# Optimization experiments

Hardware: AMD Instinct MI355X
Metric: run time of the kernel (lower is better)

Reference implementation:

```python
import jax, jax.numpy as jnp
import numpy as np

PAD_IDX = 0
EPS = 1e-5


def make_pos(L):
    # phrase[i, j] = j - i, i.e. row i is range(-i, L-i)
    phrase = (np.arange(L)[None, :] - np.arange(L)[:, None]).astype(np.float32)
    half = int(np.ceil(L / 2))
    freq = np.linspace(0.0, L, L, dtype=np.float32)[1:half]          # [F]
    pos = freq[:, None, None] * phrase[None] / L * 2.0 * np.pi       # [F, L, L]
    pos = np.concatenate([np.cos(pos), np.sin(pos)], axis=0)        # [2F, L, L]
    return jnp.asarray(np.transpose(pos, (1, 0, 2)))                # [L, P=2F, L]


def setup_inputs() -> dict:
    key = jax.random.key(0)
    ks = jax.random.split(key, 8)
    B, L, V, D, H = 2048, 64, 4096, 64, 8
    P = 2 * (int(np.ceil(L / 2)) - 1)  # 62
    inputs = jax.random.randint(ks[0], (B, L), 0, V)
    W_emb = jax.random.normal(ks[1], (V, D), jnp.float32) * 0.02
    W_emb = W_emb.at[PAD_IDX].set(0.0)  # padding_idx row is zero
    W_qkv = jax.random.normal(ks[2], (3 * H * D, D), jnp.float32) * 0.02
    W_pos = jax.random.normal(ks[3], (P, L), jnp.float32) * 0.02
    ln_g = jnp.ones((D,), jnp.float32)
    ln_b = jnp.zeros((D,), jnp.float32)
    W1 = jax.random.normal(ks[4], (64, H), jnp.float32) * 0.1
    b1 = jnp.zeros((64,), jnp.float32)
    W2 = jax.random.normal(ks[5], (32, 64), jnp.float32) * 0.1
    b2 = jnp.zeros((32,), jnp.float32)
    return dict(inputs=inputs, W_emb=W_emb, W_qkv=W_qkv, W_pos=W_pos,
                ln_g=ln_g, ln_b=ln_b, W1=W1, b1=b1, W2=W2, b2=b2,
                n_words=4, n_names=16)


def reference(inputs, W_emb, W_qkv, W_pos, ln_g, ln_b, W1, b1, W2, b2, n_words, n_names):
    B, L = inputs.shape
    V, D = W_emb.shape
    H = W_qkv.shape[0] // (3 * D)
    pos = make_pos(L)  # [L, P, L]
    P = pos.shape[1]

    # compute_qkv: per-char q/k/v tables, then gather per token.
    qkv = (W_emb @ W_qkv.T).reshape(V, 3 * H, D)
    q, k, v = qkv[:, :H], qkv[:, H:2 * H], qkv[:, 2 * H:]
    q_t = jnp.take(q, inputs, axis=0)  # [B, L, H, D]
    k_t = jnp.take(k, inputs, axis=0)
    v_t = jnp.take(v, inputs, axis=0)

    # Equivalent to gathering char_sim[h, ids, ids]: qkv is a per-token linear,
    # so q[ids] @ k[ids]^T == char_sim.index_select(1, ids).index_select(-1, ids).
    sim = jnp.einsum('blhd,bmhd->bhlm', q_t, k_t) / jnp.sqrt(jnp.float32(D))
    key_pad = (inputs == PAD_IDX)[:, None, None, :]
    sim = jnp.where(key_pad, jnp.float32(-1e9), sim)  # char_sim[:, :, pad_idx] = -1e9

    # positional bias: Linear(L->P) on clipped scores, contracted with pos basis.
    sim_clip = jnp.where(sim > -1e8, sim, jnp.float32(0.0))
    pos_w = jnp.einsum('bhlm,pm->bhlp', sim_clip, W_pos)        # [B, H, L, P]
    pos_bias = jnp.einsum('bhlp,lpm->bhlm', pos_w, pos) / P     # mean over P

    attn = jax.nn.softmax(sim + pos_bias, axis=-1)              # dropout p=0 -> id
    out = jnp.einsum('bhlm,bmhd->blhd', attn, v_t)              # [B, L, H, D]

    # sdpa LayerNorm over word_vec_d
    mu = out.mean(-1, keepdims=True)
    var = out.var(-1, keepdims=True)
    out = (out - mu) * jax.lax.rsqrt(var + EPS) * ln_g + ln_b

    # MLP over the head dimension: [B, L, D, H] -> [B, L, D, 32]
    ft = jnp.swapaxes(out, 2, 3)
    h1 = jax.nn.relu(jnp.einsum('bldh,oh->bldo', ft, W1) + b1)
    h2 = jnp.einsum('bldo,po->bldp', h1, W2) + b2
    char_ft = h2.reshape(B, L, -1)                              # [B, L, D*32]

    # masked mean pooling over chars -> word feature
    maskf = (inputs != PAD_IDX).astype(char_ft.dtype)
    word_ft = jnp.einsum('bl,blf->bf', maskf, char_ft) / maskf.sum(-1, keepdims=True)

    # equal-size splits: words -> names (mean) -> groups of names
    Fdim = word_ft.shape[-1]
    name_ft = word_ft.reshape(B // n_words, n_words, Fdim).mean(1)
    return name_ft.reshape(-1, n_names, Fdim)
```

## Files before the change

kernel.cpp:

```cpp
#include <hip/hip_runtime.h>
#include <hip/hip_bf16.h>


typedef __attribute__((ext_vector_type(8))) short short8;
typedef __attribute__((ext_vector_type(4))) float f32x4;

union FragU { uint4 u; short8 v; };

__device__ __forceinline__ unsigned short f2bf(float f) {
    union { float f; unsigned int i; } c; c.f = f;
    unsigned int i = c.i;
    unsigned int r = (i + 0x7fffu + ((i >> 16) & 1u)) >> 16;
    return (unsigned short)r;
}
__device__ __forceinline__ float asf(unsigned int u) {
    union { unsigned int i; float f; } c; c.i = u; return c.f;
}
__device__ __forceinline__ float bfsel(uint2 g, int i) {
    unsigned u = (i < 2) ? g.x : g.y;
    return asf((i & 1) ? (u & 0xffff0000u) : (u << 16));
}
__device__ __forceinline__ unsigned cvtpk(float lo, float hi) {
    unsigned r;
    asm("v_cvt_pk_bf16_f32 %0, %1, %2" : "=v"(r) : "v"(lo), "v"(hi));
    return r;
}

__device__ __forceinline__ void packstore4(unsigned* rowptr, int c,
                                           float v0, float v1, float v2, float v3) {
    float p0 = __shfl_xor(v0, 1), p1 = __shfl_xor(v1, 1);
    float p2 = __shfl_xor(v2, 1), p3 = __shfl_xor(v3, 1);
    int odd = c & 1;
    float lo0 = odd ? p2 : v0, hi0 = odd ? v2 : p0;
    float lo1 = odd ? p3 : v1, hi1 = odd ? v3 : p1;
    unsigned a0 = cvtpk(lo0, hi0);
    unsigned a1 = cvtpk(lo1, hi1);
    int ba = (c >> 1) + (odd ? 16 : 0);
    rowptr[ba] = a0; rowptr[ba + 8] = a1;
}

__device__ __forceinline__ void packline(unsigned* rowbase, int c,
                                         float v0, float v1, float v2, float v3) {
    float p0 = __shfl_xor(v0, 1), p1 = __shfl_xor(v1, 1);
    float p2 = __shfl_xor(v2, 1), p3 = __shfl_xor(v3, 1);
    int odd = c & 1;
    float lo0 = odd ? p2 : v0, hi0 = odd ? v2 : p0;
    float lo1 = odd ? p3 : v1, hi1 = odd ? v3 : p1;
    unsigned a0 = cvtpk(lo0, hi0);
    unsigned a1 = cvtpk(lo1, hi1);
    int s = (c >> 1) + (odd ? 8 : 0);
    rowbase[s] = a0; rowbase[s + 16] = a1;
}

__global__ __launch_bounds__(256) void k_qkv(const float* __restrict__ W_emb,
                                             const float* __restrict__ W_qkv,
                                             unsigned short* __restrict__ qkvb) {
    __shared__ float At[4096];
    __shared__ float Bt[4096];
    int t = threadIdx.x;
    int bt = blockIdx.x / 24, rt = blockIdx.x - bt * 24;
    int r = t >> 2, part = t & 3;
    const float4* esrc = (const float4*)(W_emb + (size_t)((bt << 6) + r) * 64 + part * 16);
    const float4* wsrc = (const float4*)(W_qkv + (size_t)((rt << 6) + r) * 64 + part * 16);
#pragma unroll
    for (int j = 0; j < 4; ++j) {
        float4 e4 = esrc[j], w4 = wsrc[j];
        int c0 = part * 16 + j * 4;
        At[(c0 + 0) * 64 + r] = e4.x; At[(c0 + 1) * 64 + r] = e4.y;
        At[(c0 + 2) * 64 + r] = e4.z; At[(c0 + 3) * 64 + r] = e4.w;
        Bt[(c0 + 0) * 64 + r] = w4.x; Bt[(c0 + 1) * 64 + r] = w4.y;
        Bt[(c0 + 2) * 64 + r] = w4.z; Bt[(c0 + 3) * 64 + r] = w4.w;
    }
    __syncthreads();
    int l0 = (t >> 4) << 2, m0 = (t & 15) << 2;
    float acc[4][4] = {};
#pragma unroll 4
    for (int k = 0; k < 64; ++k) {
        float4 a  = *(const float4*)(At + k * 64 + l0);
        float4 bb = *(const float4*)(Bt + k * 64 + m0);
        float aa[4] = {a.x, a.y, a.z, a.w};
        float bv[4] = {bb.x, bb.y, bb.z, bb.w};
#pragma unroll
        for (int i = 0; i < 4; ++i)
#pragma unroll
            for (int j = 0; j < 4; ++j)
                acc[i][j] = fmaf(aa[i], bv[j], acc[i][j]);
    }
    float qs = (rt < 8) ? 0.18033688f : 1.0f;
#pragma unroll
    for (int i = 0; i < 4; ++i) {
        unsigned w0 = (unsigned)f2bf(acc[i][0] * qs) | ((unsigned)f2bf(acc[i][1] * qs) << 16);
        unsigned w1 = (unsigned)f2bf(acc[i][2] * qs) | ((unsigned)f2bf(acc[i][3] * qs) << 16);
        unsigned* dst = (unsigned*)(qkvb + (size_t)((bt << 6) + l0 + i) * 1536 + (rt << 6) + m0);
        dst[0] = w0; dst[1] = w1;
    }
}

__global__ void k_tab(const float* __restrict__ W_pos,
                      unsigned short* __restrict__ cst,
                      unsigned short* __restrict__ csl,
                      unsigned short* __restrict__ wpos) {
    int t = threadIdx.x;
    const float w = 6.283185307179586f / 63.0f;
    for (int e = t; e < 4096; e += 256) {
        int row = e >> 6, col = e & 63;
        {
            int j = col, x = row;
            float val = 0.0f;
            if (j < 31)       val = cosf(w * (float)(((j + 1) * x) % 63));
            else if (j >= 32 && j < 63) val = sinf(w * (float)(((j - 31) * x) % 63));
            cst[e] = f2bf(val);
        }
        {
            int j = row, x = col;
            float val = 0.0f;
            if (j < 31)       val = cosf(w * (float)(((j + 1) * x) % 63));
            else if (j >= 32 && j < 63) val = sinf(w * (float)(((j - 31) * x) % 63));
            csl[e] = f2bf(val);
        }
        {
            int j = row;
            float val = 0.0f;
            if (j < 31) val = W_pos[j * 64 + col];
            else if (j >= 32 && j < 63) val = W_pos[(j - 1) * 64 + col];
            wpos[e] = f2bf(val);
        }
    }
}

__global__ __launch_bounds__(128, 4) void k_attn(
    const int* __restrict__ inputs,
    const unsigned short* __restrict__ qkvb,
    const unsigned short* __restrict__ cstg,
    const unsigned short* __restrict__ cslg,
    const unsigned short* __restrict__ wposg,
    const float* __restrict__ ln_g,
    const float* __restrict__ ln_b,
    unsigned short* __restrict__ out_n)
{
    __shared__ __align__(16) unsigned int smem[4608];
    unsigned int* S0d = smem;
    unsigned int* S1d = smem + 2304;
    int t = threadIdx.x, w2 = t >> 6, lane = t & 63;
    int b = blockIdx.x >> 3, h = blockIdx.x & 7;
    const int* toks = inputs + b * 64;
    int r = lane & 15, q = lane >> 4, c = r;
    int tk = toks[lane];
    int mt0 = 2 * w2;
    const float INV62 = 1.0f / 62.0f;

    int mk[4]; float gvv[4], bvv[4];
#pragma unroll
    for (int nt = 0; nt < 4; ++nt) {
        mk[nt] = (toks[16 * nt + c] == 0);
        gvv[nt] = ln_g[16 * nt + c];
        bvv[nt] = ln_b[16 * nt + c];
    }

    {
        const uint4* src = (const uint4*)(qkvb + (size_t)tk * 1536 + (w2 ? 512 : 0) + h * 64);
        uint4* dst = (uint4*)((w2 ? S1d : S0d) + lane * 36);
#pragma unroll
        for (int j = 0; j < 8; ++j) dst[j] = src[j];
    }
    __syncthreads();

    f32x4 sc[2][4], acc[2][4];
    const f32x4 zf = {0.f, 0.f, 0.f, 0.f};

#pragma unroll
    for (int u = 0; u < 2; ++u)
#pragma unroll
        for (int nt = 0; nt < 4; ++nt) sc[u][nt] = zf;
#pragma unroll
    for (int ks = 0; ks < 2; ++ks) {
        FragU Af[2], Bf[4];
#pragma unroll
        for (int u = 0; u < 2; ++u)
            Af[u].u = *(const uint4*)(S0d + (16 * (mt0 + u) + r) * 36 + 16 * ks + 4 * q);
#pragma unroll
        for (int nt = 0; nt < 4; ++nt)
            Bf[nt].u = *(const uint4*)(S1d + (16 * nt + r) * 36 + 16 * ks + 4 * q);
#pragma unroll
        for (int u = 0; u < 2; ++u)
#pragma unroll
            for (int nt = 0; nt < 4; ++nt)
                sc[u][nt] = __builtin_amdgcn_mfma_f32_16x16x32_bf16(Af[u].v, Bf[nt].v, sc[u][nt], 0, 0, 0);
    }
#pragma unroll
    for (int u = 0; u < 2; ++u)
#pragma unroll
        for (int i = 0; i < 4; ++i) {
            int l = 16 * (mt0 + u) + 4 * q + i;
            packstore4(S0d + l * 36, c, sc[u][0][i], sc[u][1][i], sc[u][2][i], sc[u][3][i]);
        }
    __syncthreads();

#pragma unroll
    for (int u = 0; u < 2; ++u)
#pragma unroll
        for (int nt = 0; nt < 4; ++nt) acc[u][nt] = zf;
#pragma unroll
    for (int ks = 0; ks < 2; ++ks) {
        FragU Af[2], Bf[4];
#pragma unroll
        for (int u = 0; u < 2; ++u)
            Af[u].u = *(const uint4*)(S0d + (16 * (mt0 + u) + r) * 36 + 16 * ks + 4 * q);
#pragma unroll
        for (int nt = 0; nt < 4; ++nt)
            Bf[nt].u = *(const uint4*)(wposg + (16 * nt + r) * 64 + 32 * ks + 8 * q);
#pragma unroll
        for (int u = 0; u < 2; ++u)
#pragma unroll
            for (int nt = 0; nt < 4; ++nt)
                acc[u][nt] = __builtin_amdgcn_mfma_f32_16x16x32_bf16(Af[u].v, Bf[nt].v, acc[u][nt], 0, 0, 0);
    }
#pragma unroll
    for (int u = 0; u < 2; ++u) {
        int mt = mt0 + u;
        uint2 t00 = *(const uint2*)(cslg + (c) * 64 + 16 * mt + 4 * q);
        uint2 t01 = *(const uint2*)(cslg + (32 + c) * 64 + 16 * mt + 4 * q);
        uint2 t10 = *(const uint2*)(cslg + (16 + c) * 64 + 16 * mt + 4 * q);
        uint2 t11 = *(const uint2*)(cslg + (48 + c) * 64 + 16 * mt + 4 * q);
#pragma unroll
        for (int i = 0; i < 4; ++i) {
            int l = 16 * mt + 4 * q + i;
            float cv0 = bfsel(t00, i), sv0 = bfsel(t01, i);
            float cv1 = bfsel(t10, i), sv1 = bfsel(t11, i);
            float pc0 = acc[u][0][i], ps0 = acc[u][2][i];
            float pc1 = acc[u][1][i], ps1 = acc[u][3][i];
            float u0 = pc0 * cv0 - ps0 * sv0;
            float u1 = pc1 * cv1 - ps1 * sv1;
            float u2 = pc0 * sv0 + ps0 * cv0;
            float u3 = pc1 * sv1 + ps1 * cv1;
            packstore4(S1d + l * 36, c, u0, u1, u2, u3);
        }
    }

#pragma unroll
    for (int u = 0; u < 2; ++u)
#pragma unroll
        for (int nt = 0; nt < 4; ++nt) acc[u][nt] = zf;
#pragma unroll
    for (int ks = 0; ks < 2; ++ks) {
        FragU Af[2], Bf[4];
#pragma unroll
        for (int u = 0; u < 2; ++u)
            Af[u].u = *(const uint4*)(S1d + (16 * (mt0 + u) + r) * 36 + 16 * ks + 4 * q);
#pragma unroll
        for (int nt = 0; nt < 4; ++nt)
            Bf[nt].u = *(const uint4*)(cstg + (16 * nt + r) * 64 + 32 * ks + 8 * q);
#pragma unroll
        for (int u = 0; u < 2; ++u)
#pragma unroll
            for (int nt = 0; nt < 4; ++nt)
                acc[u][nt] = __builtin_amdgcn_mfma_f32_16x16x32_bf16(Af[u].v, Bf[nt].v, acc[u][nt], 0, 0, 0);
    }

    uint4 V4[4];
    {
        const uint4* vsrc = (const uint4*)(qkvb + (size_t)tk * 1536 + 1024 + h * 64 + 32 * w2);
#pragma unroll
        for (int j = 0; j < 4; ++j) V4[j] = vsrc[j];
    }

#pragma unroll
    for (int u = 0; u < 2; ++u)
#pragma unroll
        for (int i = 0; i < 4; ++i) {
            int l = 16 * (mt0 + u) + 4 * q + i;
            float e0 = mk[0] ? 0.f : __builtin_amdgcn_exp2f(fmaf(acc[u][0][i], INV62, sc[u][0][i]));
            float e1 = mk[1] ? 0.f : __builtin_amdgcn_exp2f(fmaf(acc[u][1][i], INV62, sc[u][1][i]));
            float e2 = mk[2] ? 0.f : __builtin_amdgcn_exp2f(fmaf(acc[u][2][i], INV62, sc[u][2][i]));
            float e3 = mk[3] ? 0.f : __builtin_amdgcn_exp2f(fmaf(acc[u][3][i], INV62, sc[u][3][i]));
            float s = e0 + e1 + e2 + e3;
            s += __shfl_xor(s, 1);
            s += __shfl_xor(s, 2);
            s += __shfl_xor(s, 4);
            s += __shfl_xor(s, 8);
            float inv = __builtin_amdgcn_rcpf(s);
            packstore4(S0d + l * 36, c, e0 * inv, e1 * inv, e2 * inv, e3 * inv);
        }

    {
        int odd = lane & 1;
        const unsigned* Vd = (const unsigned*)V4;
#pragma unroll
        for (int jj = 0; jj < 16; ++jj) {
            unsigned my = Vd[jj];
            unsigned pr = __shfl_xor(my, 1);
            unsigned val = odd ? ((pr >> 16) | (my & 0xffff0000u))
                               : ((my & 0xffffu) | (pr << 16));
            S1d[(32 * w2 + 2 * jj + odd) * 36 + (lane >> 1)] = val;
        }
    }
    __syncthreads();

#pragma unroll
    for (int u = 0; u < 2; ++u)
#pragma unroll
        for (int nt = 0; nt < 4; ++nt) acc[u][nt] = zf;
#pragma unroll
    for (int ks = 0; ks < 2; ++ks) {
        FragU Af[2], Bf[4];
#pragma unroll
        for (int u = 0; u < 2; ++u)
            Af[u].u = *(const uint4*)(S0d + (16 * (mt0 + u) + r) * 36 + 16 * ks + 4 * q);
#pragma unroll
        for (int nt = 0; nt < 4; ++nt)
            Bf[nt].u = *(const uint4*)(S1d + (16 * nt + r) * 36 + 16 * ks + 4 * q);
#pragma unroll
        for (int u = 0; u < 2; ++u)
#pragma unroll
            for (int nt = 0; nt < 4; ++nt)
                acc[u][nt] = __builtin_amdgcn_mfma_f32_16x16x32_bf16(Af[u].v, Bf[nt].v, acc[u][nt], 0, 0, 0);
    }
    {
        unsigned* outw = (unsigned*)out_n;
        size_t hb = ((size_t)b * 8 + h) * 64;
#pragma unroll
        for (int u = 0; u < 2; ++u)
#pragma unroll
            for (int i = 0; i < 4; ++i) {
                int l = 16 * (mt0 + u) + 4 * q + i;
                float v0 = acc[u][0][i], v1 = acc[u][1][i], v2 = acc[u][2][i], v3 = acc[u][3][i];
                float s1 = v0 + v1 + v2 + v3;
                float s2 = v0 * v0 + v1 * v1 + v2 * v2 + v3 * v3;
                s1 += __shfl_xor(s1, 1); s2 += __shfl_xor(s2, 1);
                s1 += __shfl_xor(s1, 2); s2 += __shfl_xor(s2, 2);
                s1 += __shfl_xor(s1, 4); s2 += __shfl_xor(s2, 4);
                s1 += __shfl_xor(s1, 8); s2 += __shfl_xor(s2, 8);
                float mu = s1 * (1.0f / 64.0f);
                float var = s2 * (1.0f / 64.0f) - mu * mu;
                float rstd = __builtin_amdgcn_rsqf(var + 1e-5f);
                float cmu = -mu * rstd;
                float y0 = fmaf(fmaf(v0, rstd, cmu), gvv[0], bvv[0]);
                float y1 = fmaf(fmaf(v1, rstd, cmu), gvv[1], bvv[1]);
                float y2 = fmaf(fmaf(v2, rstd, cmu), gvv[2], bvv[2]);
                float y3 = fmaf(fmaf(v3, rstd, cmu), gvv[3], bvv[3]);
                packline(outw + (hb + l) * 32, c, y0, y1, y2, y3);
            }
    }
}

__global__ __launch_bounds__(256) void k_mlp(const int* __restrict__ inputs,
                                             const unsigned short* __restrict__ out_n,
                                             const float* __restrict__ W1,
                                             const float* __restrict__ b1,
                                             float* __restrict__ gws) {
    __shared__ unsigned short XT[8320];
    __shared__ unsigned long long vmask_s;
    __shared__ float invcnt_s;
    int t = threadIdx.x, w = t >> 6, lane = t & 63;
    int b = blockIdx.x;
    int ot = w >> 1, dt = w & 1;
    int kq = lane >> 4, n = lane & 15;

    if (t < 64) {
        int tok = inputs[b * 64 + t];
        unsigned long long bal = __ballot(tok != 0);
        if (t == 0) {
            int cnt = __popcll(bal);
            if (cnt < 1) cnt = 1;
            vmask_s = bal;
            invcnt_s = 1.0f / (float)cnt;
        }
    }

    FragU Wf[2];
#pragma unroll
    for (int om = 0; om < 2; ++om) {
        int o = 32 * ot + 16 * om + n;
        if (kq == 0) {
            const float4* wsrc = (const float4*)(W1 + o * 8);
            float4 wa = wsrc[0], wb = wsrc[1];
            Wf[om].u.x = (unsigned)f2bf(wa.x) | ((unsigned)f2bf(wa.y) << 16);
            Wf[om].u.y = (unsigned)f2bf(wa.z) | ((unsigned)f2bf(wa.w) << 16);
            Wf[om].u.z = (unsigned)f2bf(wb.x) | ((unsigned)f2bf(wb.y) << 16);
            Wf[om].u.w = (unsigned)f2bf(wb.z) | ((unsigned)f2bf(wb.w) << 16);
        } else if (kq == 1) {
            Wf[om].u = make_uint4((unsigned)f2bf(b1[o]), 0, 0, 0);
        } else {
            Wf[om].u = make_uint4(0, 0, 0, 0);
        }
    }

    f32x4 racc[2][2];
    const f32x4 zf = {0.f, 0.f, 0.f, 0.f};
#pragma unroll
    for (int dm = 0; dm < 2; ++dm)
#pragma unroll
        for (int om = 0; om < 2; ++om) racc[dm][om] = zf;

    int lh = t & 7;
    int lr = (t >> 3) & 15;
    int half = t >> 7;

    __syncthreads();
    unsigned long long vmask = vmask_s;
    float invcnt = invcnt_s;

    for (int cc = 0; cc < 4; ++cc) {
        __syncthreads();
        {
            const unsigned short* src = out_n + (size_t)b * 32768 + lh * 4096
                                        + (16 * cc + lr) * 64 + half * 32;
            unsigned short* dst = XT + lr * 520 + lh;
#pragma unroll
            for (int j = 0; j < 4; ++j) {
                uint4 u = ((const uint4*)src)[j];
                int m0 = half * 32 + j * 8;
                int d0 = (m0 >= 16 && m0 < 48) ? (m0 ^ 48) : m0;
                dst[(d0 + 0) * 8] = (unsigned short)(u.x & 0xffffu);
                dst[(d0 + 1) * 8] = (unsigned short)(u.x >> 16);
                dst[(d0 + 2) * 8] = (unsigned short)(u.y & 0xffffu);
                dst[(d0 + 3) * 8] = (unsigned short)(u.y >> 16);
                dst[(d0 + 4) * 8] = (unsigned short)(u.z & 0xffffu);
                dst[(d0 + 5) * 8] = (unsigned short)(u.z >> 16);
                dst[(d0 + 6) * 8] = (unsigned short)(u.w & 0xffffu);
                dst[(d0 + 7) * 8] = (unsigned short)(u.w >> 16);
            }
        }
        __syncthreads();
#pragma unroll 4
        for (int l = 0; l < 16; ++l) {
            if (!((vmask >> (16 * cc + l)) & 1ull)) continue;
            FragU Xf[2];
#pragma unroll
            for (int dm = 0; dm < 2; ++dm) {
                if (kq == 0)
                    Xf[dm].u = *(const uint4*)(XT + l * 520 + (32 * dt + 16 * dm + n) * 8);
                else if (kq == 1)
                    Xf[dm].u = make_uint4(0x3F80u, 0, 0, 0);
                else
                    Xf[dm].u = make_uint4(0, 0, 0, 0);
            }
#pragma unroll
            for (int dm = 0; dm < 2; ++dm)
#pragma unroll
                for (int om = 0; om < 2; ++om) {
                    f32x4 C = __builtin_amdgcn_mfma_f32_16x16x32_bf16(Xf[dm].v, Wf[om].v, zf, 0, 0, 0);
#pragma unroll
                    for (int i = 0; i < 4; ++i)
                        racc[dm][om][i] += fmaxf(C[i], 0.0f);
                }
        }
    }
    float* gb = gws + (size_t)b * 4096;
#pragma unroll
    for (int dm = 0; dm < 2; ++dm)
#pragma unroll
        for (int om = 0; om < 2; ++om) {
            int o = 32 * ot + 16 * om + n;
#pragma unroll
            for (int i = 0; i < 4; ++i) {
                int d = 32 * dt + 16 * dm + 4 * kq + i;
                gb[d * 64 + o] = racc[dm][om][i] * invcnt;
            }
        }
}

__global__ __launch_bounds__(256) void k_final(const float* __restrict__ gws,
                                               const float* __restrict__ W2,
                                               const float* __restrict__ b2,
                                               float* __restrict__ out) {
    __shared__ float gbar[4096];
    __shared__ float w2s[32 * 68];
    __shared__ float b2s[32];
    int t = threadIdx.x;
    int n = blockIdx.x;
    for (int e = t; e < 4096; e += 256) {
        size_t base = (size_t)(4 * n) * 4096 + e;
        gbar[e] = 0.25f * (gws[base] + gws[base + 4096] + gws[base + 8192] + gws[base + 12288]);
    }
    for (int e = t; e < 2048; e += 256) {
        int p = e >> 6, o = e & 63;
        w2s[p * 68 + o] = W2[e];
    }
    if (t < 32) b2s[t] = b2[t];
    __syncthreads();
#pragma unroll
    for (int jj = 0; jj < 8; ++jj) {
        int f = jj * 256 + t;
        int d = f >> 5, p = f & 31;
        float acc = b2s[p];
        for (int o4 = 0; o4 < 16; ++o4) {
            float4 gvv = *(const float4*)(gbar + d * 64 + o4 * 4);
            float4 wv = *(const float4*)(w2s + p * 68 + o4 * 4);
            acc = fmaf(gvv.x, wv.x, acc);
            acc = fmaf(gvv.y, wv.y, acc);
            acc = fmaf(gvv.z, wv.z, acc);
            acc = fmaf(gvv.w, wv.w, acc);
        }
        out[(size_t)n * 2048 + f] = acc;
    }
}

extern "C" void kernel_launch(void* const* d_in, const int* in_sizes, int n_in,
                              void* d_out, int out_size, void* d_ws, size_t ws_size,
                              hipStream_t stream) {
    const int*   inputs = (const int*)d_in[0];
    const float* W_emb  = (const float*)d_in[1];
    const float* W_qkv  = (const float*)d_in[2];
    const float* W_pos  = (const float*)d_in[3];
    const float* ln_g   = (const float*)d_in[4];
    const float* ln_b   = (const float*)d_in[5];
    const float* W1     = (const float*)d_in[6];
    const float* b1     = (const float*)d_in[7];
    const float* W2     = (const float*)d_in[8];
    const float* b2     = (const float*)d_in[9];
    float* out = (float*)d_out;

    unsigned short* qkvb = (unsigned short*)d_ws;
    unsigned short* cst  = qkvb + 6291456;
    unsigned short* csl  = cst + 4096;
    unsigned short* wpos = csl + 4096;
    float* gws = (float*)(wpos + 4096);
    unsigned short* out_n = (unsigned short*)(gws + 8388608);

    hipLaunchKernelGGL(k_qkv,   dim3(64 * 24), dim3(256), 0, stream, W_emb, W_qkv, qkvb);
    hipLaunchKernelGGL(k_tab,   dim3(1),       dim3(256), 0, stream, W_pos, cst, csl, wpos);
    hipLaunchKernelGGL(k_attn,  dim3(16384),   dim3(128), 0, stream,
                       inputs, qkvb, cst, csl, wpos, ln_g, ln_b, out_n);
    hipLaunchKernelGGL(k_mlp,   dim3(2048),    dim3(256), 0, stream, inputs, out_n, W1, b1, gws);
    hipLaunchKernelGGL(k_final, dim3(512),     dim3(256), 0, stream, gws, W2, b2, out);
}
```

Before: 355.8 us.

## Prefetch MLP transpose tiles, pair-pack LDS writes, parallelize table kernel

In the MLP kernel, the next chunk's global loads of normalized attention output are issued into registers before the current chunk's MFMA loop, hiding global latency. The LDS transpose now writes 32-bit words built by exchanging halves with the neighbouring lane via shuffle, instead of eight 16-bit scattered stores. The trig/position table kernel is spread over 16 blocks instead of a single looping block. The prefetch costs extra registers, and the shuffle-based packing depends on the lane-pair mapping being correct.

```diff
diff --git a/kernel.cpp b/kernel.cpp
--- a/kernel.cpp
+++ b/kernel.cpp
@@ -100,31 +100,29 @@
                       unsigned short* __restrict__ cst,
                       unsigned short* __restrict__ csl,
                       unsigned short* __restrict__ wpos) {
-    int t = threadIdx.x;
+    int e = blockIdx.x * 256 + threadIdx.x;
     const float w = 6.283185307179586f / 63.0f;
-    for (int e = t; e < 4096; e += 256) {
-        int row = e >> 6, col = e & 63;
-        {
-            int j = col, x = row;
-            float val = 0.0f;
-            if (j < 31)       val = cosf(w * (float)(((j + 1) * x) % 63));
-            else if (j >= 32 && j < 63) val = sinf(w * (float)(((j - 31) * x) % 63));
-            cst[e] = f2bf(val);
-        }
-        {
-            int j = row, x = col;
-            float val = 0.0f;
-            if (j < 31)       val = cosf(w * (float)(((j + 1) * x) % 63));
-            else if (j >= 32 && j < 63) val = sinf(w * (float)(((j - 31) * x) % 63));
-            csl[e] = f2bf(val);
-        }
-        {
-            int j = row;
-            float val = 0.0f;
-            if (j < 31) val = W_pos[j * 64 + col];
-            else if (j >= 32 && j < 63) val = W_pos[(j - 1) * 64 + col];
-            wpos[e] = f2bf(val);
-        }
+    int row = e >> 6, col = e & 63;
+    {
+        int j = col, x = row;
+        float val = 0.0f;
+        if (j < 31)       val = cosf(w * (float)(((j + 1) * x) % 63));
+        else if (j >= 32 && j < 63) val = sinf(w * (float)(((j - 31) * x) % 63));
+        cst[e] = f2bf(val);
+    }
+    {
+        int j = row, x = col;
+        float val = 0.0f;
+        if (j < 31)       val = cosf(w * (float)(((j + 1) * x) % 63));
+        else if (j >= 32 && j < 63) val = sinf(w * (float)(((j - 31) * x) % 63));
+        csl[e] = f2bf(val);
+    }
+    {
+        int j = row;
+        float val = 0.0f;
+        if (j < 31) val = W_pos[j * 64 + col];
+        else if (j >= 32 && j < 63) val = W_pos[(j - 1) * 64 + col];
+        wpos[e] = f2bf(val);
     }
 }
 
@@ -396,30 +394,39 @@
     int lr = (t >> 3) & 15;
     int half = t >> 7;
 
+    const uint4* src4 = (const uint4*)(out_n + (size_t)b * 32768 + lh * 4096
+                                       + lr * 64 + half * 32);
+    uint4 G[4], Gn[4];
+#pragma unroll
+    for (int j = 0; j < 4; ++j) G[j] = src4[j];
+
+    int c2 = lh >> 1, lodd = lh & 1;
+    unsigned* XTd = (unsigned*)XT;
+    int dbase = lr * 260 + c2;
+
     __syncthreads();
     unsigned long long vmask = vmask_s;
     float invcnt = invcnt_s;
 
     for (int cc = 0; cc < 4; ++cc) {
         __syncthreads();
-        {
-            const unsigned short* src = out_n + (size_t)b * 32768 + lh * 4096
-                                        + (16 * cc + lr) * 64 + half * 32;
-            unsigned short* dst = XT + lr * 520 + lh;
-#pragma unroll
-            for (int j = 0; j < 4; ++j) {
-                uint4 u = ((const uint4*)src)[j];
-                int m0 = half * 32 + j * 8;
-                int d0 = (m0 >= 16 && m0 < 48) ? (m0 ^ 48) : m0;
-                dst[(d0 + 0) * 8] = (unsigned short)(u.x & 0xffffu);
-                dst[(d0 + 1) * 8] = (unsigned short)(u.x >> 16);
-                dst[(d0 + 2) * 8] = (unsigned short)(u.y & 0xffffu);
-                dst[(d0 + 3) * 8] = (unsigned short)(u.y >> 16);
-                dst[(d0 + 4) * 8] = (unsigned short)(u.z & 0xffffu);
-                dst[(d0 + 5) * 8] = (unsigned short)(u.z >> 16);
-                dst[(d0 + 6) * 8] = (unsigned short)(u.w & 0xffffu);
-                dst[(d0 + 7) * 8] = (unsigned short)(u.w >> 16);
+#pragma unroll
+        for (int j = 0; j < 4; ++j) {
+            int m0 = half * 32 + j * 8;
+            int d0 = (m0 >= 16 && m0 < 48) ? (m0 ^ 48) : m0;
+            unsigned wv[4] = {G[j].x, G[j].y, G[j].z, G[j].w};
+#pragma unroll
+            for (int i = 0; i < 4; ++i) {
+                unsigned pw = __shfl_xor(wv[i], 1);
+                unsigned val = lodd ? ((pw >> 16) | (wv[i] & 0xffff0000u))
+                                    : ((wv[i] & 0xffffu) | (pw << 16));
+                int d = d0 + 2 * i + lodd;
+                XTd[dbase + d * 4] = val;
             }
+        }
+        if (cc < 3) {
+#pragma unroll
+            for (int j = 0; j < 4; ++j) Gn[j] = src4[(cc + 1) * 128 + j];
         }
         __syncthreads();
 #pragma unroll 4
@@ -444,6 +451,10 @@
                     for (int i = 0; i < 4; ++i)
                         racc[dm][om][i] += fmaxf(C[i], 0.0f);
                 }
+        }
+        if (cc < 3) {
+#pragma unroll
+            for (int j = 0; j < 4; ++j) G[j] = Gn[j];
         }
     }
     float* gb = gws + (size_t)b * 4096;
@@ -519,7 +530,7 @@
     unsigned short* out_n = (unsigned short*)(gws + 8388608);
 
     hipLaunchKernelGGL(k_qkv,   dim3(64 * 24), dim3(256), 0, stream, W_emb, W_qkv, qkvb);
-    hipLaunchKernelGGL(k_tab,   dim3(1),       dim3(256), 0, stream, W_pos, cst, csl, wpos);
+    hipLaunchKernelGGL(k_tab,   dim3(16),      dim3(256), 0, stream, W_pos, cst, csl, wpos);
     hipLaunchKernelGGL(k_attn,  dim3(16384),   dim3(128), 0, stream,
                        inputs, qkvb, cst, csl, wpos, ln_g, ln_b, out_n);
     hipLaunchKernelGGL(k_mlp,   dim3(2048),    dim3(256), 0, stream, inputs, out_n, W1, b1, gws);
```

New measurement: 350.2 us, median of 3. About the same (-1.6%).
